# Performance work log

Measured on AMD Instinct MI355X. Metric: run time of the kernel, lower is better.

The kernel has to match this reference:

```python
import jax, jax.numpy as jnp
import numpy as np

B, N, D = 32, 4096, 256
H, DH, S = 8, 64, 16
DI = H * DH          # dim_inner = 512
HID = 1024           # max(dim, hidden_dim)
ITERS = 3
EPS = 1e-8
SCALE = D ** (-0.5)  # NOTE: original uses dim, not dim_head


def _ln(x, g, b):
    m = jnp.mean(x, axis=-1, keepdims=True)
    v = jnp.mean((x - m) ** 2, axis=-1, keepdims=True)
    return (x - m) * jax.lax.rsqrt(v + 1e-5) * g + b


def _lin(x, W, b):  # torch layout: W [out, in]
    return x @ W.T + b


def setup_inputs() -> dict:
    key = jax.random.key(0)
    ks = jax.random.split(key, 32)

    def p(i, shape, s=0.02):
        return jax.random.normal(ks[i], shape, dtype=jnp.float32) * s

    return {
        "x": jax.random.normal(ks[0], (B, N, D), dtype=jnp.float32),
        "slots_noise": jax.random.normal(ks[1], (B, S, D), dtype=jnp.float32),
        "slots_mu": p(2, (1, 1, D), 1.0),
        "slots_logsigma": p(3, (1, 1, D)),
        "ln_in_g": jnp.ones((D,), jnp.float32), "ln_in_b": jnp.zeros((D,), jnp.float32),
        "ln_s_g": jnp.ones((D,), jnp.float32), "ln_s_b": jnp.zeros((D,), jnp.float32),
        "ln_ff_g": jnp.ones((D,), jnp.float32), "ln_ff_b": jnp.zeros((D,), jnp.float32),
        "Wq": p(4, (DI, D)), "bq": jnp.zeros((DI,), jnp.float32),
        "Wk": p(5, (DI, D)), "bk": jnp.zeros((DI,), jnp.float32),
        "Wv": p(6, (DI, D)), "bv": jnp.zeros((DI,), jnp.float32),
        "Wc": p(7, (D, DI)), "bc": jnp.zeros((D,), jnp.float32),
        "gru_wih": p(8, (3 * D, D)), "gru_whh": p(9, (3 * D, D)),
        "gru_bih": jnp.zeros((3 * D,), jnp.float32), "gru_bhh": jnp.zeros((3 * D,), jnp.float32),
        "W1": p(10, (HID, D)), "b1": jnp.zeros((HID,), jnp.float32),
        "W2": p(11, (D, HID)), "b2": jnp.zeros((D,), jnp.float32),
    }


def reference(x, slots_noise, slots_mu, slots_logsigma,
              ln_in_g, ln_in_b, ln_s_g, ln_s_b, ln_ff_g, ln_ff_b,
              Wq, bq, Wk, bk, Wv, bv, Wc, bc,
              gru_wih, gru_whh, gru_bih, gru_bhh,
              W1, b1, W2, b2):
    slots = slots_mu + jnp.exp(slots_logsigma) * slots_noise  # [B,S,D]
    xn = _ln(x, ln_in_g, ln_in_b)
    k = _lin(xn, Wk, bk).reshape(B, N, H, DH)  # [B,N,H,DH]
    v = _lin(xn, Wv, bv).reshape(B, N, H, DH)

    for _ in range(ITERS):
        slots_prev = slots
        sn = _ln(slots, ln_s_g, ln_s_b)
        q = _lin(sn, Wq, bq).reshape(B, S, H, DH)             # [B,S,H,DH]
        logits = jnp.einsum('bihd,bjhd->bhij', q, k) * SCALE  # [B,H,S,N]
        attn = jax.nn.softmax(logits, axis=-1) + EPS
        attn = attn / jnp.sum(attn, axis=-1, keepdims=True)
        upd = jnp.einsum('bhij,bjhd->bihd', attn, v).reshape(B, S, DI)
        upd = _lin(upd, Wc, bc)                               # [B,S,D]
        # GRUCell (torch gate order r, z, n)
        gi = _lin(upd.reshape(-1, D), gru_wih, gru_bih)
        gh = _lin(slots_prev.reshape(-1, D), gru_whh, gru_bhh)
        ir, iz, inn = jnp.split(gi, 3, axis=-1)
        hr, hz, hn = jnp.split(gh, 3, axis=-1)
        r = jax.nn.sigmoid(ir + hr)
        z = jax.nn.sigmoid(iz + hz)
        n = jnp.tanh(inn + r * hn)
        slots = ((1.0 - z) * n + z * slots_prev.reshape(-1, D)).reshape(B, S, D)
        slots = slots + _lin(jax.nn.relu(_lin(_ln(slots, ln_ff_g, ln_ff_b), W1, b1)), W2, b2)
    return slots
```

## Files before the change

### kernel.cpp

```cpp
#include <hip/hip_runtime.h>
#include <stdint.h>

#define B_   32
#define N_   4096
#define D_   256
#define H_   8
#define S_   16
#define DI_  512
#define HID_ 1024
#define CH_  8
#define NCHUNK_ 512
#define SCALE_ 0.0625f

typedef short  short8 __attribute__((ext_vector_type(8)));
typedef float  f32x4  __attribute__((ext_vector_type(4)));

__device__ __forceinline__ unsigned short f2bf(float x){
  union { float f; unsigned u; } v; v.f = x;
  unsigned r = v.u + 0x7FFFu + ((v.u >> 16) & 1u);
  return (unsigned short)(r >> 16);
}

__device__ __forceinline__ void gld16(const void* g, void* l){
  __builtin_amdgcn_global_load_lds(
      (const __attribute__((address_space(1))) unsigned int*)g,
      (__attribute__((address_space(3))) unsigned int*)l, 16, 0, 0);
}

#define FMA4(acc, a, Wm) do { (acc)[0] += (a)*(Wm).x; (acc)[1] += (a)*(Wm).y; (acc)[2] += (a)*(Wm).z; (acc)[3] += (a)*(Wm).w; } while(0)

__global__ void k_badws(float* out){ out[blockIdx.x*256 + threadIdx.x] = 1e9f; }

__global__ __launch_bounds__(256) void k_init_slots(
    const float* __restrict__ noise, const float* __restrict__ mu,
    const float* __restrict__ lsig, float* __restrict__ slots)
{
  int i = blockIdx.x*256 + threadIdx.x;
  int d = i & 255;
  slots[i] = mu[d] + expf(lsig[d]) * noise[i];
}

__global__ __launch_bounds__(256) void k_transpose(
    const float* __restrict__ src, float* __restrict__ dst, int R, int C)
{
  __shared__ float t[32][33];
  int c0 = blockIdx.x*32, r0 = blockIdx.y*32;
  int tx = threadIdx.x, ty = threadIdx.y;
  for (int j = 0; j < 32; j += 8){
    int r = r0 + ty + j, c = c0 + tx;
    if (r < R && c < C) t[ty+j][tx] = src[(size_t)r*C + c];
  }
  __syncthreads();
  for (int j = 0; j < 32; j += 8){
    int c = c0 + ty + j, r = r0 + tx;
    if (c < C && r < R) dst[(size_t)c*R + r] = t[tx][ty+j];
  }
}

__global__ __launch_bounds__(256) void k_ln_x(
    const float* __restrict__ x, const float* __restrict__ g, const float* __restrict__ bb,
    unsigned short* __restrict__ xn, unsigned short* __restrict__ xnT)
{
  __shared__ __align__(16) char tile[32768];
  const int blk = blockIdx.x;
  const int b  = blk >> 6;
  const int n0 = (blk & 63) * 64;
  const int t = threadIdx.x;
  const int lane = t & 63;
  const int w = t >> 6;
  float4 gv = *(const float4*)&g[lane*4];
  float4 bv = *(const float4*)&bb[lane*4];
#pragma unroll 1
  for (int it = 0; it < 16; ++it){
    const int nl = w*16 + it;
    const size_t row = (size_t)b*N_ + n0 + nl;
    float4 xv = *(const float4*)&x[row*256 + lane*4];
    float s = xv.x + xv.y + xv.z + xv.w;
    float q = xv.x*xv.x + xv.y*xv.y + xv.z*xv.z + xv.w*xv.w;
#pragma unroll
    for (int m = 1; m < 64; m <<= 1){ s += __shfl_xor(s, m); q += __shfl_xor(q, m); }
    float mean = s * 0.00390625f;
    float var  = q * 0.00390625f - mean*mean;
    float rs = rsqrtf(var + 1e-5f);
    unsigned short u0 = f2bf((xv.x-mean)*rs*gv.x + bv.x);
    unsigned short u1 = f2bf((xv.y-mean)*rs*gv.y + bv.y);
    unsigned short u2 = f2bf((xv.z-mean)*rs*gv.z + bv.z);
    unsigned short u3 = f2bf((xv.w-mean)*rs*gv.w + bv.w);
    uint2 pk; pk.x = (unsigned)u0 | ((unsigned)u1 << 16); pk.y = (unsigned)u2 | ((unsigned)u3 << 16);
    *(uint2*)&xn[row*256 + lane*4] = pk;
    *(uint2*)(tile + nl*512 + ((lane*8) ^ ((nl & 7) << 4))) = pk;
  }
  __syncthreads();
  {
    unsigned dw[32];
    const int cp  = lane >> 1;
    const int par = lane & 1;
#pragma unroll
    for (int i = 0; i < 32; ++i){
      int nl = 2*i + par;
      unsigned v = *(const unsigned*)(tile + nl*512 + ((w*128 + cp*4) ^ ((nl & 7) << 4)));
      unsigned o = __shfl_xor(v, 1);
      unsigned lo = par ? o : v;
      unsigned hi = par ? v : o;
      dw[i] = par ? ((lo >> 16) | (hi & 0xffff0000u))
                  : ((lo & 0xffffu) | (hi << 16));
    }
    const int d = w*64 + lane;
    unsigned short* dst = &xnT[((size_t)b*D_ + d)*N_ + n0];
#pragma unroll
    for (int j = 0; j < 8; ++j)
      *(uint4*)(dst + j*8) = *(const uint4*)&dw[j*4];
  }
}

__global__ __launch_bounds__(256) void k_preA(
    const float* __restrict__ slots, const float* __restrict__ lsg, const float* __restrict__ lsb,
    const float* __restrict__ WqT, const float* __restrict__ bq, float* __restrict__ ql)
{
  __shared__ __align__(16) float a[4][256];
  const int lane = threadIdx.x & 63, w = threadIdx.x >> 6;
  const int row = blockIdx.x*4 + w;
  const int o   = blockIdx.y*64 + lane;
  float4 v = *(const float4*)&slots[(size_t)row*D_ + lane*4];
  float s = v.x + v.y + v.z + v.w;
  float q = v.x*v.x + v.y*v.y + v.z*v.z + v.w*v.w;
#pragma unroll
  for (int m = 1; m < 64; m <<= 1){ s += __shfl_xor(s, m); q += __shfl_xor(q, m); }
  float mean = s * 0.00390625f;
  float var  = q * 0.00390625f - mean*mean;
  float rs = rsqrtf(var + 1e-5f);
  float4 gv = *(const float4*)&lsg[lane*4];
  float4 bv = *(const float4*)&lsb[lane*4];
  a[w][lane*4+0] = (v.x-mean)*rs*gv.x + bv.x;
  a[w][lane*4+1] = (v.y-mean)*rs*gv.y + bv.y;
  a[w][lane*4+2] = (v.z-mean)*rs*gv.z + bv.z;
  a[w][lane*4+3] = (v.w-mean)*rs*gv.w + bv.w;
  const float* Wp = WqT + o;
  float acc = 0.f;
#pragma unroll 4
  for (int k4 = 0; k4 < 64; ++k4){
    float4 av = *(const float4*)&a[w][k4*4];
    acc += av.x * Wp[(size_t)(k4*4+0)*512];
    acc += av.y * Wp[(size_t)(k4*4+1)*512];
    acc += av.z * Wp[(size_t)(k4*4+2)*512];
    acc += av.w * Wp[(size_t)(k4*4+3)*512];
  }
  ql[(size_t)row*DI_ + o] = acc + bq[o];
}

__global__ __launch_bounds__(256) void k_preB(
    const float* __restrict__ ql, const float* __restrict__ Wk, const float* __restrict__ bk,
    unsigned short* __restrict__ qp, float* __restrict__ qb)
{
  __shared__ __align__(16) float qs[16][64];
  const int id = blockIdx.x;
  const int b  = id >> 3;
  const int h  = id & 7;
  const int cb = blockIdx.y;
  const int c0 = cb*64;
  const int t = threadIdx.x;
  const int lane = t & 63, w = t >> 6;
  {
    int flat = t*4;
    int s = flat >> 6, k = flat & 63;
    *(float4*)&qs[s][k] = *(const float4*)&ql[((size_t)(b*S_ + s))*DI_ + h*64 + k];
  }
  __syncthreads();
  if (cb == 0){
    float bkv = bk[h*64 + lane];
#pragma unroll
    for (int r = 0; r < 4; ++r){
      int s = w*4 + r;
      float v = qs[s][lane] * bkv;
#pragma unroll
      for (int m = 1; m < 64; m <<= 1) v += __shfl_xor(v, m);
      if (lane == 0) qb[((size_t)b*H_ + h)*S_ + s] = v * SCALE_;
    }
  }
  float acc[4] = {};
  const float* Wp = Wk + (size_t)(h*64)*256 + c0 + lane;
#pragma unroll 4
  for (int k = 0; k < 64; ++k){
    float wv = Wp[(size_t)k*256];
    acc[0] += qs[w*4+0][k] * wv;
    acc[1] += qs[w*4+1][k] * wv;
    acc[2] += qs[w*4+2][k] * wv;
    acc[3] += qs[w*4+3][k] * wv;
  }
#pragma unroll
  for (int r = 0; r < 4; ++r){
    int s = w*4 + r;
    qp[(((size_t)b*H_ + h)*S_ + s)*D_ + c0 + lane] = f2bf(SCALE_ * acc[r]);
  }
}

__global__ __launch_bounds__(512, 2) void k_flash(
    const unsigned short* __restrict__ xn, const unsigned short* __restrict__ xnT,
    const unsigned short* __restrict__ qp, const float* __restrict__ qb,
    float* __restrict__ mPart, float* __restrict__ lPart, float* __restrict__ axPart)
{
  __shared__ __align__(16) char lds[147456];
  const int ch = blockIdx.x;
  const int b  = blockIdx.y;
  const int t  = threadIdx.x;
  const int lane = t & 63;
  const int w  = t >> 6;
  const int g  = lane >> 4;
  const int c  = lane & 15;
  const int n0 = ch * NCHUNK_;

  short8 aq[8];
#pragma unroll
  for (int ks = 0; ks < 8; ++ks)
    aq[ks] = *(const short8*)&qp[(((size_t)b*H_ + w)*S_ + c)*D_ + ks*32 + g*8];
  float qbr[4];
#pragma unroll
  for (int r = 0; r < 4; ++r)
    qbr[r] = qb[((size_t)b*H_ + w)*S_ + g*4 + r];

  f32x4 accX[16];
#pragma unroll
  for (int i = 0; i < 16; ++i){ f32x4 z = {0.f,0.f,0.f,0.f}; accX[i] = z; }
  float mrun[4] = {-1e30f,-1e30f,-1e30f,-1e30f};
  float lrun[4] = {0.f,0.f,0.f,0.f};

  auto ISSUE = [&](int tl, int buf){
    char* lb = lds + buf*65536;
#pragma unroll
    for (int j = 0; j < 4; ++j){
      int rl = w*8 + j*2 + (lane >> 5);
      int cs = (lane & 31) ^ (rl & 7);
      gld16(&xn[((size_t)b*N_ + n0 + tl*64 + rl)*D_ + cs*8],
            lb + (w*8 + j*2)*512);
    }
#pragma unroll
    for (int j = 0; j < 4; ++j){
      int dl = w*32 + j*8 + (lane >> 3);
      int cs = (lane & 7) ^ (dl & 7);
      gld16(&xnT[((size_t)b*D_ + dl)*N_ + n0 + tl*64 + cs*8],
            lb + 32768 + (w*32 + j*8)*128);
    }
  };

  ISSUE(0, 0);
  __syncthreads();
  int cur = 0;
#pragma unroll 1
  for (int tl = 0; tl < 8; ++tl){
    if (tl < 7) ISSUE(tl + 1, cur ^ 1);
    const char* xb  = lds + cur*65536;
    const char* xbT = lds + cur*65536 + 32768;
    char* pbuf = lds + 131072 + w*2048;
    f32x4 lg[4];
#pragma unroll
    for (int nf = 0; nf < 4; ++nf){ f32x4 z = {0.f,0.f,0.f,0.f}; lg[nf] = z; }
#pragma unroll
    for (int ks = 0; ks < 8; ++ks){
#pragma unroll
      for (int nf = 0; nf < 4; ++nf){
        int n = nf*16 + c;
        short8 bf = *(const short8*)(xb + n*512 + (((ks*32 + g*8)*2) ^ ((n & 7) << 4)));
        lg[nf] = __builtin_amdgcn_mfma_f32_16x16x32_bf16(aq[ks], bf, lg[nf], 0, 0, 0);
      }
    }
    float tmax[4];
#pragma unroll
    for (int r = 0; r < 4; ++r){
      lg[0][r] += qbr[r]; lg[1][r] += qbr[r]; lg[2][r] += qbr[r]; lg[3][r] += qbr[r];
      tmax[r] = fmaxf(fmaxf(lg[0][r], lg[1][r]), fmaxf(lg[2][r], lg[3][r]));
      tmax[r] = fmaxf(tmax[r], __shfl_xor(tmax[r], 1));
      tmax[r] = fmaxf(tmax[r], __shfl_xor(tmax[r], 2));
      tmax[r] = fmaxf(tmax[r], __shfl_xor(tmax[r], 4));
      tmax[r] = fmaxf(tmax[r], __shfl_xor(tmax[r], 8));
    }
    float fac[4], psum[4];
#pragma unroll
    for (int r = 0; r < 4; ++r){
      float mnew = fmaxf(mrun[r], tmax[r]);
      fac[r] = __expf(mrun[r] - mnew);
      mrun[r] = mnew;
      lrun[r] *= fac[r];
      psum[r] = 0.f;
    }
#pragma unroll
    for (int i = 0; i < 16; ++i){
      accX[i][0] *= fac[0]; accX[i][1] *= fac[1]; accX[i][2] *= fac[2]; accX[i][3] *= fac[3];
    }
#pragma unroll
    for (int nf = 0; nf < 4; ++nf){
#pragma unroll
      for (int r = 0; r < 4; ++r){
        float p = __expf(lg[nf][r] - mrun[r]);
        psum[r] += p;
        int row = g*4 + r;
        *(unsigned short*)(pbuf + row*128 + (((nf*16 + c)*2) ^ ((row & 7) << 4))) = f2bf(p);
      }
    }
#pragma unroll
    for (int r = 0; r < 4; ++r){
      psum[r] += __shfl_xor(psum[r], 1);
      psum[r] += __shfl_xor(psum[r], 2);
      psum[r] += __shfl_xor(psum[r], 4);
      psum[r] += __shfl_xor(psum[r], 8);
      lrun[r] += psum[r];
    }
#pragma unroll
    for (int ks = 0; ks < 2; ++ks){
      short8 pa = *(const short8*)(pbuf + c*128 + (((ks*32 + g*8)*2) ^ ((c & 7) << 4)));
#pragma unroll
      for (int df = 0; df < 16; ++df){
        int d = df*16 + c;
        short8 bt = *(const short8*)(xbT + d*128 + (((ks*32 + g*8)*2) ^ ((d & 7) << 4)));
        accX[df] = __builtin_amdgcn_mfma_f32_16x16x32_bf16(pa, bt, accX[df], 0, 0, 0);
      }
    }
    __syncthreads();
    cur ^= 1;
  }
  size_t base = (((size_t)b*CH_ + ch)*H_ + w)*S_;
  if (c == 0){
#pragma unroll
    for (int r = 0; r < 4; ++r){
      mPart[base + g*4 + r] = mrun[r];
      lPart[base + g*4 + r] = lrun[r];
    }
  }
  size_t base3 = base * D_;
#pragma unroll
  for (int df = 0; df < 16; ++df){
#pragma unroll
    for (int r = 0; r < 4; ++r){
      axPart[base3 + df*256 + r*64 + lane] = accX[df][r];
    }
  }
}

__global__ __launch_bounds__(256) void k_combine(
    const float* __restrict__ mPart, const float* __restrict__ lPart, const float* __restrict__ axPart,
    const float* __restrict__ WvT, const float* __restrict__ bv, float* __restrict__ upd)
{
  __shared__ __align__(16) float av[4][256];
  const int id = blockIdx.x;
  const int b  = id >> 5;
  const int h  = (id >> 2) & 7;
  const int sq = id & 3;
  const int t = threadIdx.x;
  const int sl = t >> 6;
  const int lane = t & 63;
  const int s = sq*4 + sl;
  const int sg = s >> 2, sr = s & 3;
  const size_t pb = (((size_t)b*CH_)*H_ + h)*S_ + s;
  float mg = -1e30f;
  float mv[8], lv[8];
#pragma unroll
  for (int k = 0; k < 8; ++k){
    mv[k] = mPart[pb + (size_t)k*128];
    lv[k] = lPart[pb + (size_t)k*128];
    mg = fmaxf(mg, mv[k]);
  }
  const size_t off_s = (size_t)sr*64 + sg*16 + (lane>>2)*256 + (lane&3)*4;
  float L = 0.f, ax0 = 0.f, ax1 = 0.f, ax2 = 0.f, ax3 = 0.f;
#pragma unroll
  for (int k = 0; k < 8; ++k){
    float wgt = __expf(mv[k] - mg);
    L += lv[k]*wgt;
    size_t base3 = ((((size_t)b*CH_ + k)*H_ + h)*S_) * D_;
    float4 a4 = *(const float4*)&axPart[base3 + off_s];
    ax0 += a4.x*wgt; ax1 += a4.y*wgt; ax2 += a4.z*wgt; ax3 += a4.w*wgt;
  }
  float inv = 1.f / L;
  av[sl][lane*4+0] = ax0*inv; av[sl][lane*4+1] = ax1*inv;
  av[sl][lane*4+2] = ax2*inv; av[sl][lane*4+3] = ax3*inv;
  __syncthreads();
  float acc = bv[h*64 + lane];
  for (int d = 0; d < 256; d += 2){
    float2 a2 = *(const float2*)&av[sl][d];
    acc += a2.x * WvT[(size_t)d*512     + h*64 + lane];
    acc += a2.y * WvT[(size_t)(d+1)*512 + h*64 + lane];
  }
  upd[((size_t)b*S_ + s)*DI_ + h*64 + lane] = acc;
}

__global__ __launch_bounds__(256) void k_sA(
    const float* __restrict__ upd, const float* __restrict__ WcT,
    const float* __restrict__ bc, float* __restrict__ updc)
{
  __shared__ __align__(16) float act[4][512];
  const int lane = threadIdx.x & 63, w = threadIdx.x >> 6;
  const int row = blockIdx.x*4 + w;
  const int col = blockIdx.y*64 + lane;
  *(float4*)&act[w][lane*8]     = *(const float4*)&upd[(size_t)row*DI_ + lane*8];
  *(float4*)&act[w][lane*8 + 4] = *(const float4*)&upd[(size_t)row*DI_ + lane*8 + 4];
  const float* Wp = WcT + col;
  float acc = 0.f;
#pragma unroll 4
  for (int k4 = 0; k4 < 128; ++k4){
    float4 a = *(const float4*)&act[w][k4*4];
    acc += a.x * Wp[(size_t)(k4*4+0)*256];
    acc += a.y * Wp[(size_t)(k4*4+1)*256];
    acc += a.z * Wp[(size_t)(k4*4+2)*256];
    acc += a.w * Wp[(size_t)(k4*4+3)*256];
  }
  updc[(size_t)row*D_ + col] = acc + bc[col];
}

__global__ __launch_bounds__(256) void k_sB(
    const float* __restrict__ updc, const float* __restrict__ slots,
    const float* __restrict__ wihT, const float* __restrict__ whhT,
    const float* __restrict__ bih, const float* __restrict__ bhh,
    float* __restrict__ snl)
{
  __shared__ __align__(16) float au[4][256];
  __shared__ __align__(16) float as[4][256];
  const int lane = threadIdx.x & 63, w = threadIdx.x >> 6;
  const int row = blockIdx.x*4 + w;
  const int d   = blockIdx.y*64 + lane;
  *(float4*)&au[w][lane*4] = *(const float4*)&updc[(size_t)row*D_ + lane*4];
  *(float4*)&as[w][lane*4] = *(const float4*)&slots[(size_t)row*D_ + lane*4];
  const float* Wi = wihT + d;
  const float* Wh = whhT + d;
  float air=0.f, aiz=0.f, ain=0.f, ahr=0.f, ahz=0.f, ahn=0.f;
#pragma unroll 2
  for (int k4 = 0; k4 < 64; ++k4){
    float4 u = *(const float4*)&au[w][k4*4];
    float4 s = *(const float4*)&as[w][k4*4];
#pragma unroll
    for (int j = 0; j < 4; ++j){
      int k = k4*4 + j;
      float uv = (j==0)?u.x:(j==1)?u.y:(j==2)?u.z:u.w;
      float sv = (j==0)?s.x:(j==1)?s.y:(j==2)?s.z:s.w;
      air += uv * Wi[(size_t)k*768];
      aiz += uv * Wi[(size_t)k*768 + 256];
      ain += uv * Wi[(size_t)k*768 + 512];
      ahr += sv * Wh[(size_t)k*768];
      ahz += sv * Wh[(size_t)k*768 + 256];
      ahn += sv * Wh[(size_t)k*768 + 512];
    }
  }
  float ir = air + bih[d]     + ahr + bhh[d];
  float iz = aiz + bih[256+d] + ahz + bhh[256+d];
  float rg = 1.f/(1.f + __expf(-ir));
  float zg = 1.f/(1.f + __expf(-iz));
  float ng = tanhf(ain + bih[512+d] + rg*(ahn + bhh[512+d]));
  snl[(size_t)row*D_ + d] = (1.f - zg)*ng + zg*as[w][d];
}

__global__ __launch_bounds__(256) void k_sC(
    const float* __restrict__ snl, const float* __restrict__ lfg, const float* __restrict__ lfb,
    const float* __restrict__ W1T, const float* __restrict__ b1, float* __restrict__ h1)
{
  __shared__ __align__(16) float a[4][256];
  const int lane = threadIdx.x & 63, w = threadIdx.x >> 6;
  const int row = blockIdx.x*4 + w;
  const int o   = blockIdx.y*64 + lane;
  float4 v = *(const float4*)&snl[(size_t)row*D_ + lane*4];
  float s = v.x + v.y + v.z + v.w;
  float q = v.x*v.x + v.y*v.y + v.z*v.z + v.w*v.w;
#pragma unroll
  for (int m = 1; m < 64; m <<= 1){ s += __shfl_xor(s, m); q += __shfl_xor(q, m); }
  float mean = s * 0.00390625f;
  float var  = q * 0.00390625f - mean*mean;
  float rs = rsqrtf(var + 1e-5f);
  float4 gv = *(const float4*)&lfg[lane*4];
  float4 bv = *(const float4*)&lfb[lane*4];
  a[w][lane*4+0] = (v.x-mean)*rs*gv.x + bv.x;
  a[w][lane*4+1] = (v.y-mean)*rs*gv.y + bv.y;
  a[w][lane*4+2] = (v.z-mean)*rs*gv.z + bv.z;
  a[w][lane*4+3] = (v.w-mean)*rs*gv.w + bv.w;
  const float* Wp = W1T + o;
  float acc = 0.f;
#pragma unroll 4
  for (int k4 = 0; k4 < 64; ++k4){
    float4 av = *(const float4*)&a[w][k4*4];
    acc += av.x * Wp[(size_t)(k4*4+0)*1024];
    acc += av.y * Wp[(size_t)(k4*4+1)*1024];
    acc += av.z * Wp[(size_t)(k4*4+2)*1024];
    acc += av.w * Wp[(size_t)(k4*4+3)*1024];
  }
  h1[(size_t)row*HID_ + o] = fmaxf(acc + b1[o], 0.f);
}

__global__ __launch_bounds__(256) void k_sD(
    const float* __restrict__ h1, const float* __restrict__ snl,
    const float* __restrict__ W2T, const float* __restrict__ b2, float* __restrict__ dst)
{
  __shared__ __align__(16) float a[4][1024];
  const int lane = threadIdx.x & 63, w = threadIdx.x >> 6;
  const int row = blockIdx.x*4 + w;
  const int o   = blockIdx.y*64 + lane;
#pragma unroll
  for (int j = 0; j < 4; ++j)
    *(float4*)&a[w][lane*16 + j*4] = *(const float4*)&h1[(size_t)row*HID_ + lane*16 + j*4];
  const float* Wp = W2T + o;
  float acc = 0.f;
#pragma unroll 4
  for (int k4 = 0; k4 < 256; ++k4){
    float4 av = *(const float4*)&a[w][k4*4];
    acc += av.x * Wp[(size_t)(k4*4+0)*256];
    acc += av.y * Wp[(size_t)(k4*4+1)*256];
    acc += av.z * Wp[(size_t)(k4*4+2)*256];
    acc += av.w * Wp[(size_t)(k4*4+3)*256];
  }
  dst[(size_t)row*D_ + o] = snl[(size_t)row*D_ + o] + acc + b2[o];
}

extern "C" void kernel_launch(void* const* d_in, const int* in_sizes, int n_in,
                              void* d_out, int out_size, void* d_ws, size_t ws_size,
                              hipStream_t stream)
{
  const float* x       = (const float*)d_in[0];
  const float* noise   = (const float*)d_in[1];
  const float* mu      = (const float*)d_in[2];
  const float* lsig    = (const float*)d_in[3];
  const float* ln_in_g = (const float*)d_in[4];
  const float* ln_in_b = (const float*)d_in[5];
  const float* ln_s_g  = (const float*)d_in[6];
  const float* ln_s_b  = (const float*)d_in[7];
  const float* ln_ff_g = (const float*)d_in[8];
  const float* ln_ff_b = (const float*)d_in[9];
  const float* Wq  = (const float*)d_in[10]; const float* bq  = (const float*)d_in[11];
  const float* Wk  = (const float*)d_in[12]; const float* bk  = (const float*)d_in[13];
  const float* Wv  = (const float*)d_in[14]; const float* bv  = (const float*)d_in[15];
  const float* Wc  = (const float*)d_in[16]; const float* bc  = (const float*)d_in[17];
  const float* wih = (const float*)d_in[18]; const float* whh = (const float*)d_in[19];
  const float* bih = (const float*)d_in[20]; const float* bhh = (const float*)d_in[21];
  const float* W1  = (const float*)d_in[22]; const float* b1  = (const float*)d_in[23];
  const float* W2  = (const float*)d_in[24]; const float* b2  = (const float*)d_in[25];

  char* ws = (char*)d_ws;
  unsigned short* xn  = (unsigned short*)(ws + 0);
  unsigned short* xnT = (unsigned short*)(ws + 67108864);
  float* slots = (float*)(ws + 134217728);
  unsigned short* qp = (unsigned short*)(ws + 134742016);
  float* qb   = (float*)(ws + 136839168);
  float* mP   = (float*)(ws + 136855552);
  float* lP   = (float*)(ws + 136986624);
  float* axP  = (float*)(ws + 137117696);
  float* upd  = (float*)(ws + 170672128);
  float* WqT  = (float*)(ws + 171720704);
  float* WvT  = (float*)(ws + 172244992);
  float* WcT  = (float*)(ws + 172769280);
  float* wihT = (float*)(ws + 173293568);
  float* whhT = (float*)(ws + 174080000);
  float* W1T  = (float*)(ws + 174866432);
  float* W2T  = (float*)(ws + 175915008);
  float* updc = (float*)(ws + 137117696);
  float* snl  = (float*)(ws + 137641984);
  float* h1   = (float*)(ws + 138166272);
  float* ql   = (float*)(ws + 141000704);

  if (ws_size < (size_t)176963584ull){
    k_badws<<<512, 256, 0, stream>>>((float*)d_out);
    return;
  }

  k_init_slots<<<512, 256, 0, stream>>>(noise, mu, lsig, slots);
  k_ln_x<<<2048, 256, 0, stream>>>(x, ln_in_g, ln_in_b, xn, xnT);
  dim3 tb(32, 8);
  k_transpose<<<dim3(8, 16), tb, 0, stream>>>(Wq,  WqT,  512,  256);
  k_transpose<<<dim3(8, 16), tb, 0, stream>>>(Wv,  WvT,  512,  256);
  k_transpose<<<dim3(16, 8), tb, 0, stream>>>(Wc,  WcT,  256,  512);
  k_transpose<<<dim3(8, 24), tb, 0, stream>>>(wih, wihT, 768,  256);
  k_transpose<<<dim3(8, 24), tb, 0, stream>>>(whh, whhT, 768,  256);
  k_transpose<<<dim3(8, 32), tb, 0, stream>>>(W1,  W1T,  1024, 256);
  k_transpose<<<dim3(32, 8), tb, 0, stream>>>(W2,  W2T,  256,  1024);

  for (int it = 0; it < 3; ++it){
    k_preA<<<dim3(128, 8), 256, 0, stream>>>(slots, ln_s_g, ln_s_b, WqT, bq, ql);
    k_preB<<<dim3(256, 4), 256, 0, stream>>>(ql, Wk, bk, qp, qb);
    k_flash<<<dim3(CH_, B_), 512, 0, stream>>>(xn, xnT, qp, qb, mP, lP, axP);
    k_combine<<<1024, 256, 0, stream>>>(mP, lP, axP, WvT, bv, upd);
    k_sA<<<dim3(128, 4),  256, 0, stream>>>(upd, WcT, bc, updc);
    k_sB<<<dim3(128, 4),  256, 0, stream>>>(updc, slots, wihT, whhT, bih, bhh, snl);
    k_sC<<<dim3(128, 16), 256, 0, stream>>>(snl, ln_ff_g, ln_ff_b, W1T, b1, h1);
    k_sD<<<dim3(128, 4),  256, 0, stream>>>(h1, snl, W2T, b2, (it == 2) ? (float*)d_out : slots);
  }
}
```

Measured before the change: 584.9 us.

## Transpose xn tiles in LDS inside flash kernel instead of storing xnT

```diff
diff --git a/kernel.cpp b/kernel.cpp
--- a/kernel.cpp
+++ b/kernel.cpp
@@ -8,8 +8,8 @@
 #define S_   16
 #define DI_  512
 #define HID_ 1024
-#define CH_  8
-#define NCHUNK_ 512
+#define CH_  16
+#define NCHUNK_ 256
 #define SCALE_ 0.0625f
 
 typedef short  short8 __attribute__((ext_vector_type(8)));
@@ -27,8 +27,6 @@
       (__attribute__((address_space(3))) unsigned int*)l, 16, 0, 0);
 }
 
-#define FMA4(acc, a, Wm) do { (acc)[0] += (a)*(Wm).x; (acc)[1] += (a)*(Wm).y; (acc)[2] += (a)*(Wm).z; (acc)[3] += (a)*(Wm).w; } while(0)
-
 __global__ void k_badws(float* out){ out[blockIdx.x*256 + threadIdx.x] = 1e9f; }
 
 __global__ __launch_bounds__(256) void k_init_slots(
@@ -40,11 +38,25 @@
   slots[i] = mu[d] + expf(lsig[d]) * noise[i];
 }
 
-__global__ __launch_bounds__(256) void k_transpose(
-    const float* __restrict__ src, float* __restrict__ dst, int R, int C)
+__global__ __launch_bounds__(256) void k_tr_all(
+    const float* __restrict__ Wq,  const float* __restrict__ Wv,  const float* __restrict__ Wc,
+    const float* __restrict__ wih, const float* __restrict__ whh,
+    const float* __restrict__ W1,  const float* __restrict__ W2,
+    float* __restrict__ WqT, float* __restrict__ WvT, float* __restrict__ WcT,
+    float* __restrict__ wihT, float* __restrict__ whhT,
+    float* __restrict__ W1T, float* __restrict__ W2T)
 {
   __shared__ float t[32][33];
-  int c0 = blockIdx.x*32, r0 = blockIdx.y*32;
+  const int id = blockIdx.x;
+  const float* src; float* dst; int R, C, bx, by;
+  if      (id < 128) { src=Wq;  dst=WqT;  R=512;  C=256;  int s=id;      bx=s&7;  by=s>>3; }
+  else if (id < 256) { src=Wv;  dst=WvT;  R=512;  C=256;  int s=id-128;  bx=s&7;  by=s>>3; }
+  else if (id < 384) { src=Wc;  dst=WcT;  R=256;  C=512;  int s=id-256;  bx=s&15; by=s>>4; }
+  else if (id < 576) { src=wih; dst=wihT; R=768;  C=256;  int s=id-384;  bx=s&7;  by=s>>3; }
+  else if (id < 768) { src=whh; dst=whhT; R=768;  C=256;  int s=id-576;  bx=s&7;  by=s>>3; }
+  else if (id < 1024){ src=W1;  dst=W1T;  R=1024; C=256;  int s=id-768;  bx=s&7;  by=s>>3; }
+  else               { src=W2;  dst=W2T;  R=256;  C=1024; int s=id-1024; bx=s&31; by=s>>5; }
+  int c0 = bx*32, r0 = by*32;
   int tx = threadIdx.x, ty = threadIdx.y;
   for (int j = 0; j < 32; j += 8){
     int r = r0 + ty + j, c = c0 + tx;
@@ -59,9 +71,8 @@
 
 __global__ __launch_bounds__(256) void k_ln_x(
     const float* __restrict__ x, const float* __restrict__ g, const float* __restrict__ bb,
-    unsigned short* __restrict__ xn, unsigned short* __restrict__ xnT)
-{
-  __shared__ __align__(16) char tile[32768];
+    unsigned short* __restrict__ xn)
+{
   const int blk = blockIdx.x;
   const int b  = blk >> 6;
   const int n0 = (blk & 63) * 64;
@@ -88,28 +99,6 @@
     unsigned short u3 = f2bf((xv.w-mean)*rs*gv.w + bv.w);
     uint2 pk; pk.x = (unsigned)u0 | ((unsigned)u1 << 16); pk.y = (unsigned)u2 | ((unsigned)u3 << 16);
     *(uint2*)&xn[row*256 + lane*4] = pk;
-    *(uint2*)(tile + nl*512 + ((lane*8) ^ ((nl & 7) << 4))) = pk;
-  }
-  __syncthreads();
-  {
-    unsigned dw[32];
-    const int cp  = lane >> 1;
-    const int par = lane & 1;
-#pragma unroll
-    for (int i = 0; i < 32; ++i){
-      int nl = 2*i + par;
-      unsigned v = *(const unsigned*)(tile + nl*512 + ((w*128 + cp*4) ^ ((nl & 7) << 4)));
-      unsigned o = __shfl_xor(v, 1);
-      unsigned lo = par ? o : v;
-      unsigned hi = par ? v : o;
-      dw[i] = par ? ((lo >> 16) | (hi & 0xffff0000u))
-                  : ((lo & 0xffffu) | (hi << 16));
-    }
-    const int d = w*64 + lane;
-    unsigned short* dst = &xnT[((size_t)b*D_ + d)*N_ + n0];
-#pragma unroll
-    for (int j = 0; j < 8; ++j)
-      *(uint4*)(dst + j*8) = *(const uint4*)&dw[j*4];
   }
 }
 
@@ -194,12 +183,12 @@
   }
 }
 
-__global__ __launch_bounds__(512, 2) void k_flash(
-    const unsigned short* __restrict__ xn, const unsigned short* __restrict__ xnT,
+__global__ __launch_bounds__(512, 4) void k_flash(
+    const unsigned short* __restrict__ xn,
     const unsigned short* __restrict__ qp, const float* __restrict__ qb,
     float* __restrict__ mPart, float* __restrict__ lPart, float* __restrict__ axPart)
 {
-  __shared__ __align__(16) char lds[147456];
+  __shared__ __align__(16) char lds[57344];
   const int ch = blockIdx.x;
   const int b  = blockIdx.y;
   const int t  = threadIdx.x;
@@ -225,39 +214,31 @@
   float lrun[4] = {0.f,0.f,0.f,0.f};
 
   auto ISSUE = [&](int tl, int buf){
-    char* lb = lds + buf*65536;
-#pragma unroll
-    for (int j = 0; j < 4; ++j){
-      int rl = w*8 + j*2 + (lane >> 5);
+    char* lb = lds + buf*16384;
+#pragma unroll
+    for (int j = 0; j < 2; ++j){
+      int rl = w*4 + j*2 + (lane >> 5);
       int cs = (lane & 31) ^ (rl & 7);
-      gld16(&xn[((size_t)b*N_ + n0 + tl*64 + rl)*D_ + cs*8],
-            lb + (w*8 + j*2)*512);
-    }
-#pragma unroll
-    for (int j = 0; j < 4; ++j){
-      int dl = w*32 + j*8 + (lane >> 3);
-      int cs = (lane & 7) ^ (dl & 7);
-      gld16(&xnT[((size_t)b*D_ + dl)*N_ + n0 + tl*64 + cs*8],
-            lb + 32768 + (w*32 + j*8)*128);
+      gld16(&xn[((size_t)b*N_ + n0 + tl*32 + rl)*D_ + cs*8],
+            lb + (w*4 + j*2)*512);
     }
   };
 
   ISSUE(0, 0);
   __syncthreads();
   int cur = 0;
+  char* pbuf = lds + 49152 + w*1024;
 #pragma unroll 1
   for (int tl = 0; tl < 8; ++tl){
     if (tl < 7) ISSUE(tl + 1, cur ^ 1);
-    const char* xb  = lds + cur*65536;
-    const char* xbT = lds + cur*65536 + 32768;
-    char* pbuf = lds + 131072 + w*2048;
-    f32x4 lg[4];
-#pragma unroll
-    for (int nf = 0; nf < 4; ++nf){ f32x4 z = {0.f,0.f,0.f,0.f}; lg[nf] = z; }
+    const char* xb = lds + cur*16384;
+    f32x4 lg[2];
+#pragma unroll
+    for (int nf = 0; nf < 2; ++nf){ f32x4 z = {0.f,0.f,0.f,0.f}; lg[nf] = z; }
 #pragma unroll
     for (int ks = 0; ks < 8; ++ks){
 #pragma unroll
-      for (int nf = 0; nf < 4; ++nf){
+      for (int nf = 0; nf < 2; ++nf){
         int n = nf*16 + c;
         short8 bf = *(const short8*)(xb + n*512 + (((ks*32 + g*8)*2) ^ ((n & 7) << 4)));
         lg[nf] = __builtin_amdgcn_mfma_f32_16x16x32_bf16(aq[ks], bf, lg[nf], 0, 0, 0);
@@ -266,8 +247,8 @@
     float tmax[4];
 #pragma unroll
     for (int r = 0; r < 4; ++r){
-      lg[0][r] += qbr[r]; lg[1][r] += qbr[r]; lg[2][r] += qbr[r]; lg[3][r] += qbr[r];
-      tmax[r] = fmaxf(fmaxf(lg[0][r], lg[1][r]), fmaxf(lg[2][r], lg[3][r]));
+      lg[0][r] += qbr[r]; lg[1][r] += qbr[r];
+      tmax[r] = fmaxf(lg[0][r], lg[1][r]);
       tmax[r] = fmaxf(tmax[r], __shfl_xor(tmax[r], 1));
       tmax[r] = fmaxf(tmax[r], __shfl_xor(tmax[r], 2));
       tmax[r] = fmaxf(tmax[r], __shfl_xor(tmax[r], 4));
@@ -287,13 +268,13 @@
       accX[i][0] *= fac[0]; accX[i][1] *= fac[1]; accX[i][2] *= fac[2]; accX[i][3] *= fac[3];
     }
 #pragma unroll
-    for (int nf = 0; nf < 4; ++nf){
+    for (int nf = 0; nf < 2; ++nf){
 #pragma unroll
       for (int r = 0; r < 4; ++r){
         float p = __expf(lg[nf][r] - mrun[r]);
         psum[r] += p;
         int row = g*4 + r;
-        *(unsigned short*)(pbuf + row*128 + (((nf*16 + c)*2) ^ ((row & 7) << 4))) = f2bf(p);
+        *(unsigned short*)(pbuf + row*64 + (((nf*16 + c)*2) ^ ((row & 3) << 4))) = f2bf(p);
       }
     }
 #pragma unroll
@@ -304,13 +285,32 @@
       psum[r] += __shfl_xor(psum[r], 8);
       lrun[r] += psum[r];
     }
-#pragma unroll
-    for (int ks = 0; ks < 2; ++ks){
-      short8 pa = *(const short8*)(pbuf + c*128 + (((ks*32 + g*8)*2) ^ ((c & 7) << 4)));
+    {
+      const int par = lane & 1;
+      const int cp  = (lane >> 1) & 15;
+      const int hh  = lane >> 5;
+      unsigned dwv[8];
+#pragma unroll
+      for (int i = 0; i < 8; ++i){
+        int nl = hh*16 + 2*i + par;
+        unsigned v = *(const unsigned*)(xb + nl*512 + ((w*64 + cp*4) ^ ((nl & 7) << 4)));
+        unsigned o = __shfl_xor(v, 1);
+        unsigned lo = par ? o : v;
+        unsigned hi = par ? v : o;
+        dwv[i] = par ? ((lo >> 16) | (hi & 0xffff0000u))
+                     : ((lo & 0xffffu) | (hi << 16));
+      }
+      int d = w*32 + (lane & 31);
+      *(uint4*)(lds + 32768 + d*64 + (((hh*2    )*16) ^ ((d & 3) << 4))) = *(const uint4*)&dwv[0];
+      *(uint4*)(lds + 32768 + d*64 + (((hh*2 + 1)*16) ^ ((d & 3) << 4))) = *(const uint4*)&dwv[4];
+    }
+    __syncthreads();
+    {
+      short8 pa = *(const short8*)(pbuf + c*64 + ((g*16) ^ ((c & 3) << 4)));
 #pragma unroll
       for (int df = 0; df < 16; ++df){
-        int d = df*16 + c;
-        short8 bt = *(const short8*)(xbT + d*128 + (((ks*32 + g*8)*2) ^ ((d & 7) << 4)));
+        int d2 = df*16 + c;
+        short8 bt = *(const short8*)(lds + 32768 + d2*64 + ((g*16) ^ ((d2 & 3) << 4)));
         accX[df] = __builtin_amdgcn_mfma_f32_16x16x32_bf16(pa, bt, accX[df], 0, 0, 0);
       }
     }
@@ -351,17 +351,17 @@
   const int sg = s >> 2, sr = s & 3;
   const size_t pb = (((size_t)b*CH_)*H_ + h)*S_ + s;
   float mg = -1e30f;
-  float mv[8], lv[8];
-#pragma unroll
-  for (int k = 0; k < 8; ++k){
-    mv[k] = mPart[pb + (size_t)k*128];
-    lv[k] = lPart[pb + (size_t)k*128];
+  float mv[CH_], lv[CH_];
+#pragma unroll
+  for (int k = 0; k < CH_; ++k){
+    mv[k] = mPart[pb + (size_t)k*(H_*S_)];
+    lv[k] = lPart[pb + (size_t)k*(H_*S_)];
     mg = fmaxf(mg, mv[k]);
   }
   const size_t off_s = (size_t)sr*64 + sg*16 + (lane>>2)*256 + (lane&3)*4;
   float L = 0.f, ax0 = 0.f, ax1 = 0.f, ax2 = 0.f, ax3 = 0.f;
 #pragma unroll
-  for (int k = 0; k < 8; ++k){
+  for (int k = 0; k < CH_; ++k){
     float wgt = __expf(mv[k] - mg);
     L += lv[k]*wgt;
     size_t base3 = ((((size_t)b*CH_ + k)*H_ + h)*S_) * D_;
@@ -528,47 +528,40 @@
   const float* W2  = (const float*)d_in[24]; const float* b2  = (const float*)d_in[25];
 
   char* ws = (char*)d_ws;
-  unsigned short* xn  = (unsigned short*)(ws + 0);
-  unsigned short* xnT = (unsigned short*)(ws + 67108864);
-  float* slots = (float*)(ws + 134217728);
-  unsigned short* qp = (unsigned short*)(ws + 134742016);
-  float* qb   = (float*)(ws + 136839168);
-  float* mP   = (float*)(ws + 136855552);
-  float* lP   = (float*)(ws + 136986624);
-  float* axP  = (float*)(ws + 137117696);
-  float* upd  = (float*)(ws + 170672128);
-  float* WqT  = (float*)(ws + 171720704);
-  float* WvT  = (float*)(ws + 172244992);
-  float* WcT  = (float*)(ws + 172769280);
-  float* wihT = (float*)(ws + 173293568);
-  float* whhT = (float*)(ws + 174080000);
-  float* W1T  = (float*)(ws + 174866432);
-  float* W2T  = (float*)(ws + 175915008);
-  float* updc = (float*)(ws + 137117696);
-  float* snl  = (float*)(ws + 137641984);
-  float* h1   = (float*)(ws + 138166272);
-  float* ql   = (float*)(ws + 141000704);
-
-  if (ws_size < (size_t)176963584ull){
+  unsigned short* xn = (unsigned short*)(ws + 0);
+  float* slots = (float*)(ws + 67108864);
+  unsigned short* qp = (unsigned short*)(ws + 67633152);
+  float* qb   = (float*)(ws + 69730304);
+  float* mP   = (float*)(ws + 69746688);
+  float* lP   = (float*)(ws + 70008832);
+  float* axP  = (float*)(ws + 70270976);
+  float* upd  = (float*)(ws + 137379840);
+  float* WqT  = (float*)(ws + 138428416);
+  float* WvT  = (float*)(ws + 138952704);
+  float* WcT  = (float*)(ws + 139476992);
+  float* wihT = (float*)(ws + 140001280);
+  float* whhT = (float*)(ws + 140787712);
+  float* W1T  = (float*)(ws + 141574144);
+  float* W2T  = (float*)(ws + 142622720);
+  float* updc = (float*)(ws + 70270976);
+  float* snl  = (float*)(ws + 70795264);
+  float* h1   = (float*)(ws + 71319552);
+  float* ql   = (float*)(ws + 73416704);
+
+  if (ws_size < (size_t)143671296ull){
     k_badws<<<512, 256, 0, stream>>>((float*)d_out);
     return;
   }
 
   k_init_slots<<<512, 256, 0, stream>>>(noise, mu, lsig, slots);
-  k_ln_x<<<2048, 256, 0, stream>>>(x, ln_in_g, ln_in_b, xn, xnT);
-  dim3 tb(32, 8);
-  k_transpose<<<dim3(8, 16), tb, 0, stream>>>(Wq,  WqT,  512,  256);
-  k_transpose<<<dim3(8, 16), tb, 0, stream>>>(Wv,  WvT,  512,  256);
-  k_transpose<<<dim3(16, 8), tb, 0, stream>>>(Wc,  WcT,  256,  512);
-  k_transpose<<<dim3(8, 24), tb, 0, stream>>>(wih, wihT, 768,  256);
-  k_transpose<<<dim3(8, 24), tb, 0, stream>>>(whh, whhT, 768,  256);
-  k_transpose<<<dim3(8, 32), tb, 0, stream>>>(W1,  W1T,  1024, 256);
-  k_transpose<<<dim3(32, 8), tb, 0, stream>>>(W2,  W2T,  256,  1024);
+  k_ln_x<<<2048, 256, 0, stream>>>(x, ln_in_g, ln_in_b, xn);
+  k_tr_all<<<1280, dim3(32, 8), 0, stream>>>(Wq, Wv, Wc, wih, whh, W1, W2,
+                                             WqT, WvT, WcT, wihT, whhT, W1T, W2T);
 
   for (int it = 0; it < 3; ++it){
     k_preA<<<dim3(128, 8), 256, 0, stream>>>(slots, ln_s_g, ln_s_b, WqT, bq, ql);
     k_preB<<<dim3(256, 4), 256, 0, stream>>>(ql, Wk, bk, qp, qb);
-    k_flash<<<dim3(CH_, B_), 512, 0, stream>>>(xn, xnT, qp, qb, mP, lP, axP);
+    k_flash<<<dim3(CH_, B_), 512, 0, stream>>>(xn, qp, qb, mP, lP, axP);
     k_combine<<<1024, 256, 0, stream>>>(mP, lP, axP, WvT, bv, upd);
     k_sA<<<dim3(128, 4),  256, 0, stream>>>(upd, WcT, bc, updc);
     k_sB<<<dim3(128, 4),  256, 0, stream>>>(updc, slots, wihT, whhT, bih, bhh, snl);
```

New measurement: 760.4 us. +30.0%, slower.
